# Kernel tuning notes

Measured on AMD Instinct MI355X. Metric: run time of the kernel, lower is better.

Reference implementation:

```python
import jax, jax.numpy as jnp
from jax import lax
import numpy as np

WIN = 9          # window size per spatial dim (default [9]*ndims)
PAD = WIN // 2
EPS = 1e-07


def _box_sum(x, groups):
    # depthwise conv with all-ones kernel == sliding-window sum
    kernel = jnp.ones((groups, 1, WIN, WIN), dtype=x.dtype)
    return lax.conv_general_dilated(
        x, kernel,
        window_strides=(1, 1),
        padding=[(PAD, PAD), (PAD, PAD)],
        feature_group_count=groups,
        dimension_numbers=('NCHW', 'OIHW', 'NCHW'))


def setup_inputs() -> dict:
    key = jax.random.key(0)
    k1, k2 = jax.random.split(key)
    shape = (8, 1, 1024, 1024)
    y_pred = jax.random.normal(k1, shape, dtype=jnp.float32)
    y_true = jax.random.normal(k2, shape, dtype=jnp.float32)
    return {"y_pred": y_pred, "y_true": y_true}


def reference(y_pred, y_true):
    Ii = y_true
    Ji = y_pred
    groups = Ii.shape[1]
    win_size = float(WIN * WIN)

    I_sum = _box_sum(Ii, groups)
    J_sum = _box_sum(Ji, groups)
    I2_sum = _box_sum(Ii * Ii, groups)
    J2_sum = _box_sum(Ji * Ji, groups)
    IJ_sum = _box_sum(Ii * Ji, groups)

    u_I = I_sum / win_size
    u_J = J_sum / win_size
    cross = IJ_sum / win_size - u_I * u_J
    I_var = I2_sum / win_size - u_I * u_I
    J_var = J2_sum / win_size - u_J * u_J

    cc = cross / jnp.sqrt(jnp.maximum(I_var * J_var, EPS))
    return 1.0 - jnp.mean(cc)
```

## Files before the change

### kernel.cpp

```cpp
#include <hip/hip_runtime.h>

#define H 1024
#define W 1024
#define TY 8
#define NT 64
#define RS 10
#define PCOL 264
#define NBK 64

__global__ void ncc_zero(double* acc) {
    if (threadIdx.x < NBK) acc[threadIdx.x] = 0.0;
}

__global__ void ncc_finalize(const double* __restrict__ acc, float* __restrict__ out) {
    double s = 0.0;
    #pragma unroll
    for (int i = 0; i < NBK; ++i) s += acc[i];
    out[0] = 1.0f - (float)(s * (1.0 / 8388608.0));
}

__device__ __forceinline__ unsigned pk2(float lo, float hi) {
    unsigned r;
    asm("v_cvt_pk_bf16_f32 %0, %1, %2" : "=v"(r) : "v"(lo), "v"(hi));
    return r;
}
__device__ __forceinline__ float ulo(unsigned u) { return __uint_as_float(u << 16); }
__device__ __forceinline__ float uhi(unsigned u) { return __uint_as_float(u & 0xffff0000u); }

__global__ __launch_bounds__(NT) void ncc_main(
    const float* __restrict__ Jg,
    const float* __restrict__ Ig,
    double* __restrict__ acc)
{
    __shared__ unsigned short ring[RS][2][PCOL];

    const int n     = blockIdx.x;
    const int b     = n & 7;
    const int rest  = n >> 3;
    const int panel = rest & 3;
    const int strip = rest >> 2;
    const int y0    = strip * TY;
    const int lane  = threadIdx.x;
    const int wb    = panel << 8;
    const int x0    = wb + (lane << 2);
    const int p0    = lane << 2;
    const int pown  = p0 + 4;

    const float* __restrict__ Ib = Ig + (size_t)b * (H * W);
    const float* __restrict__ Jb = Jg + (size_t)b * (H * W);

    const bool  hl  = (lane < 4);
    const int   hx  = (lane < 2) ? (wb - 4) : (wb + 256);
    const float mhx = (hl && (unsigned)hx <= (unsigned)(W - 4)) ? 1.0f : 0.0f;
    const int   hxc = min(max(hx, 0), W - 4);
    const float* hbase = (lane & 1) ? Jb : Ib;
    const int   hp  = (lane < 2) ? 0 : 260;
    const int   him = lane & 1;

    float rI[4]={0,0,0,0}, rJ[4]={0,0,0,0}, rII[4]={0,0,0,0}, rJJ[4]={0,0,0,0}, rIJ[4]={0,0,0,0};
    float accv = 0.0f;
    const float inv = 1.0f / 81.0f;

    float4 Pi, Pj, Ph = {0, 0, 0, 0};
    float  Pm;

#define FLOAD(yy) do {                                                              \
        const int r_ = (yy);                                                        \
        Pm = ((unsigned)r_ < (unsigned)H) ? 1.0f : 0.0f;                            \
        const int rc_ = min(max(r_, 0), H - 1);                                     \
        Pi = *(const float4*)(Ib + (size_t)rc_ * W + x0);                           \
        Pj = *(const float4*)(Jb + (size_t)rc_ * W + x0);                           \
        if (hl) Ph = *(const float4*)(hbase + (size_t)rc_ * W + hxc);               \
    } while (0)

#define PACKW(sl) do {                                                              \
        const unsigned i01_ = pk2(Pi.x * Pm, Pi.y * Pm);                            \
        const unsigned i23_ = pk2(Pi.z * Pm, Pi.w * Pm);                            \
        const unsigned j01_ = pk2(Pj.x * Pm, Pj.y * Pm);                            \
        const unsigned j23_ = pk2(Pj.z * Pm, Pj.w * Pm);                            \
        *(uint2*)&ring[sl][0][pown] = make_uint2(i01_, i23_);                       \
        *(uint2*)&ring[sl][1][pown] = make_uint2(j01_, j23_);                       \
        if (hl) {                                                                   \
            const float mm_ = Pm * mhx;                                             \
            const unsigned h01_ = pk2(Ph.x * mm_, Ph.y * mm_);                      \
            const unsigned h23_ = pk2(Ph.z * mm_, Ph.w * mm_);                      \
            *(uint2*)&ring[sl][him][hp] = make_uint2(h01_, h23_);                   \
        }                                                                           \
    } while (0)

#define READS(sl, A, B, C, D, E, F) do {                                            \
        A = *(const uint2*)&ring[sl][0][p0];                                        \
        B = *(const uint2*)&ring[sl][0][p0 + 4];                                    \
        C = *(const uint2*)&ring[sl][0][p0 + 8];                                    \
        D = *(const uint2*)&ring[sl][1][p0];                                        \
        E = *(const uint2*)&ring[sl][1][p0 + 4];                                    \
        F = *(const uint2*)&ring[sl][1][p0 + 8];                                    \
    } while (0)

#define FOLD12(Ua, Ub, Uc, Va, Vb, Vc, SG) do {                                     \
        const float i0=ulo(Ua.x), i1=uhi(Ua.x), i2=ulo(Ua.y), i3=uhi(Ua.y);         \
        const float i4=ulo(Ub.x), i5=uhi(Ub.x), i6=ulo(Ub.y), i7=uhi(Ub.y);         \
        const float i8=ulo(Uc.x), i9=uhi(Uc.x), i10=ulo(Uc.y), i11=uhi(Uc.y);       \
        const float j0=ulo(Va.x), j1=uhi(Va.x), j2=ulo(Va.y), j3=uhi(Va.y);         \
        const float j4=ulo(Vb.x), j5=uhi(Vb.x), j6=ulo(Vb.y), j7=uhi(Vb.y);         \
        const float j8=ulo(Vc.x), j9=uhi(Vc.x), j10=ulo(Vc.y), j11=uhi(Vc.y);       \
        { float s_ = i0+i1+i2+i3+i4+i5+i6+i7+i8;                                    \
          rI[0] += SG*s_; s_ += i9-i0;  rI[1] += SG*s_;                             \
          s_ += i10-i1;   rI[2] += SG*s_; s_ += i11-i2; rI[3] += SG*s_; }           \
        { float s_ = j0+j1+j2+j3+j4+j5+j6+j7+j8;                                    \
          rJ[0] += SG*s_; s_ += j9-j0;  rJ[1] += SG*s_;                             \
          s_ += j10-j1;   rJ[2] += SG*s_; s_ += j11-j2; rJ[3] += SG*s_; }           \
        { const float q0=i0*i0,q1=i1*i1,q2=i2*i2,q3=i3*i3,q4=i4*i4,q5=i5*i5;        \
          const float q6=i6*i6,q7=i7*i7,q8=i8*i8,q9=i9*i9,q10=i10*i10,q11=i11*i11;  \
          float s_ = q0+q1+q2+q3+q4+q5+q6+q7+q8;                                    \
          rII[0] += SG*s_; s_ += q9-q0;  rII[1] += SG*s_;                           \
          s_ += q10-q1;    rII[2] += SG*s_; s_ += q11-q2; rII[3] += SG*s_; }        \
        { const float q0=j0*j0,q1=j1*j1,q2=j2*j2,q3=j3*j3,q4=j4*j4,q5=j5*j5;        \
          const float q6=j6*j6,q7=j7*j7,q8=j8*j8,q9=j9*j9,q10=j10*j10,q11=j11*j11;  \
          float s_ = q0+q1+q2+q3+q4+q5+q6+q7+q8;                                    \
          rJJ[0] += SG*s_; s_ += q9-q0;  rJJ[1] += SG*s_;                           \
          s_ += q10-q1;    rJJ[2] += SG*s_; s_ += q11-q2; rJJ[3] += SG*s_; }        \
        { const float q0=i0*j0,q1=i1*j1,q2=i2*j2,q3=i3*j3,q4=i4*j4,q5=i5*j5;        \
          const float q6=i6*j6,q7=i7*j7,q8=i8*j8,q9=i9*j9,q10=i10*j10,q11=i11*j11;  \
          float s_ = q0+q1+q2+q3+q4+q5+q6+q7+q8;                                    \
          rIJ[0] += SG*s_; s_ += q9-q0;  rIJ[1] += SG*s_;                           \
          s_ += q10-q1;    rIJ[2] += SG*s_; s_ += q11-q2; rIJ[3] += SG*s_; }        \
    } while (0)

#define CC() do {                                                                   \
        _Pragma("unroll")                                                           \
        for (int c = 0; c < 4; ++c) {                                               \
            const float uI    = rI[c] * inv;                                        \
            const float uJ    = rJ[c] * inv;                                        \
            const float cross = rIJ[c] * inv - uI * uJ;                             \
            const float Iv    = rII[c] * inv - uI * uI;                             \
            const float Jv    = rJJ[c] * inv - uJ * uJ;                             \
            accv += cross * rsqrtf(fmaxf(Iv * Jv, 1e-7f));                          \
        }                                                                           \
    } while (0)

    FLOAD(y0 - 4);
    #pragma unroll 1
    for (int r = 0; r < 9; ++r) {
        PACKW(r);
        asm volatile("" ::: "memory");
        uint2 Ua, Ub, Uc, Va, Vb, Vc;
        READS(r, Ua, Ub, Uc, Va, Vb, Vc);
        asm volatile("" ::: "memory");
        FLOAD(y0 - 3 + r);
        FOLD12(Ua, Ub, Uc, Va, Vb, Vc, 1.0f);
    }

    int ls = 0, es = 9;
    #pragma unroll 1
    for (int k = 0; k < TY - 1; ++k) {
        PACKW(es);
        asm volatile("" ::: "memory");
        uint2 eUa, eUb, eUc, eVa, eVb, eVc;
        uint2 lUa, lUb, lUc, lVa, lVb, lVc;
        READS(es, eUa, eUb, eUc, eVa, eVb, eVc);
        READS(ls, lUa, lUb, lUc, lVa, lVb, lVc);
        asm volatile("" ::: "memory");
        FLOAD(y0 + 6 + k);
        CC();
        FOLD12(eUa, eUb, eUc, eVa, eVb, eVc,  1.0f);
        FOLD12(lUa, lUb, lUc, lVa, lVb, lVc, -1.0f);
        ls += 1;
        es = (es == RS - 1) ? 0 : es + 1;
    }
    CC();

#undef CC
#undef FOLD12
#undef READS
#undef PACKW
#undef FLOAD

    #pragma unroll
    for (int off = 32; off > 0; off >>= 1)
        accv += __shfl_down(accv, off);
    if (lane == 0)
        atomicAdd(&acc[n & (NBK - 1)], (double)accv);
}

extern "C" void kernel_launch(void* const* d_in, const int* in_sizes, int n_in,
                              void* d_out, int out_size, void* d_ws, size_t ws_size,
                              hipStream_t stream) {
    const float* y_pred = (const float*)d_in[0];
    const float* y_true = (const float*)d_in[1];
    float* out = (float*)d_out;
    double* accp = (double*)d_ws;

    ncc_zero<<<dim3(1), dim3(NBK), 0, stream>>>(accp);
    ncc_main<<<dim3(8 * 4 * (H / TY)), dim3(NT), 0, stream>>>(y_pred, y_true, accp);
    ncc_finalize<<<dim3(1), dim3(1), 0, stream>>>(accp, out);
}
```

Before: 46.25 us.

## Interleave I/J bf16 in uint4 LDS groups and double rows per block

Each ring slot now packs the I and J bf16 values for four columns into one uint4. A thread reads its 12-column window with three 16-byte LDS loads instead of six 8-byte loads, and each halo lane now loads both images. Rows per block go from 8 to 16, which halves the fraction of 9-row warm-up reads and folds per output row. The leaving-row index now wraps around the ring, which the longer loop needs. The trade-off is half as many blocks and a longer serial loop per wavefront.

```diff
diff --git a/kernel.cpp b/kernel.cpp
--- a/kernel.cpp
+++ b/kernel.cpp
@@ -2,10 +2,10 @@
 
 #define H 1024
 #define W 1024
-#define TY 8
+#define TY 16
 #define NT 64
 #define RS 10
-#define PCOL 264
+#define NG 66
 #define NBK 64
 
 __global__ void ncc_zero(double* acc) {
@@ -32,7 +32,7 @@
     const float* __restrict__ Ig,
     double* __restrict__ acc)
 {
-    __shared__ unsigned short ring[RS][2][PCOL];
+    __shared__ uint4 ring[RS][NG];
 
     const int n     = blockIdx.x;
     const int b     = n & 7;
@@ -43,25 +43,21 @@
     const int lane  = threadIdx.x;
     const int wb    = panel << 8;
     const int x0    = wb + (lane << 2);
-    const int p0    = lane << 2;
-    const int pown  = p0 + 4;
 
     const float* __restrict__ Ib = Ig + (size_t)b * (H * W);
     const float* __restrict__ Jb = Jg + (size_t)b * (H * W);
 
-    const bool  hl  = (lane < 4);
-    const int   hx  = (lane < 2) ? (wb - 4) : (wb + 256);
+    const bool  hl  = (lane < 2);
+    const int   hx  = (lane == 0) ? (wb - 4) : (wb + 256);
     const float mhx = (hl && (unsigned)hx <= (unsigned)(W - 4)) ? 1.0f : 0.0f;
     const int   hxc = min(max(hx, 0), W - 4);
-    const float* hbase = (lane & 1) ? Jb : Ib;
-    const int   hp  = (lane < 2) ? 0 : 260;
-    const int   him = lane & 1;
+    const int   hg  = (lane == 0) ? 0 : (NG - 1);
 
     float rI[4]={0,0,0,0}, rJ[4]={0,0,0,0}, rII[4]={0,0,0,0}, rJJ[4]={0,0,0,0}, rIJ[4]={0,0,0,0};
     float accv = 0.0f;
     const float inv = 1.0f / 81.0f;
 
-    float4 Pi, Pj, Ph = {0, 0, 0, 0};
+    float4 Pi, Pj, Phi = {0,0,0,0}, Phj = {0,0,0,0};
     float  Pm;
 
 #define FLOAD(yy) do {                                                              \
@@ -70,40 +66,43 @@
         const int rc_ = min(max(r_, 0), H - 1);                                     \
         Pi = *(const float4*)(Ib + (size_t)rc_ * W + x0);                           \
         Pj = *(const float4*)(Jb + (size_t)rc_ * W + x0);                           \
-        if (hl) Ph = *(const float4*)(hbase + (size_t)rc_ * W + hxc);               \
+        if (hl) {                                                                   \
+            Phi = *(const float4*)(Ib + (size_t)rc_ * W + hxc);                     \
+            Phj = *(const float4*)(Jb + (size_t)rc_ * W + hxc);                     \
+        }                                                                           \
     } while (0)
 
 #define PACKW(sl) do {                                                              \
-        const unsigned i01_ = pk2(Pi.x * Pm, Pi.y * Pm);                            \
-        const unsigned i23_ = pk2(Pi.z * Pm, Pi.w * Pm);                            \
-        const unsigned j01_ = pk2(Pj.x * Pm, Pj.y * Pm);                            \
-        const unsigned j23_ = pk2(Pj.z * Pm, Pj.w * Pm);                            \
-        *(uint2*)&ring[sl][0][pown] = make_uint2(i01_, i23_);                       \
-        *(uint2*)&ring[sl][1][pown] = make_uint2(j01_, j23_);                       \
+        uint4 v_;                                                                   \
+        v_.x = pk2(Pi.x * Pm, Pi.y * Pm);                                           \
+        v_.y = pk2(Pi.z * Pm, Pi.w * Pm);                                           \
+        v_.z = pk2(Pj.x * Pm, Pj.y * Pm);                                           \
+        v_.w = pk2(Pj.z * Pm, Pj.w * Pm);                                           \
+        ring[sl][lane + 1] = v_;                                                    \
         if (hl) {                                                                   \
             const float mm_ = Pm * mhx;                                             \
-            const unsigned h01_ = pk2(Ph.x * mm_, Ph.y * mm_);                      \
-            const unsigned h23_ = pk2(Ph.z * mm_, Ph.w * mm_);                      \
-            *(uint2*)&ring[sl][him][hp] = make_uint2(h01_, h23_);                   \
+            uint4 h_;                                                               \
+            h_.x = pk2(Phi.x * mm_, Phi.y * mm_);                                   \
+            h_.y = pk2(Phi.z * mm_, Phi.w * mm_);                                   \
+            h_.z = pk2(Phj.x * mm_, Phj.y * mm_);                                   \
+            h_.w = pk2(Phj.z * mm_, Phj.w * mm_);                                   \
+            ring[sl][hg] = h_;                                                      \
         }                                                                           \
     } while (0)
 
-#define READS(sl, A, B, C, D, E, F) do {                                            \
-        A = *(const uint2*)&ring[sl][0][p0];                                        \
-        B = *(const uint2*)&ring[sl][0][p0 + 4];                                    \
-        C = *(const uint2*)&ring[sl][0][p0 + 8];                                    \
-        D = *(const uint2*)&ring[sl][1][p0];                                        \
-        E = *(const uint2*)&ring[sl][1][p0 + 4];                                    \
-        F = *(const uint2*)&ring[sl][1][p0 + 8];                                    \
+#define READS(sl, G0, G1, G2) do {                                                  \
+        G0 = ring[sl][lane];                                                        \
+        G1 = ring[sl][lane + 1];                                                    \
+        G2 = ring[sl][lane + 2];                                                    \
     } while (0)
 
-#define FOLD12(Ua, Ub, Uc, Va, Vb, Vc, SG) do {                                     \
-        const float i0=ulo(Ua.x), i1=uhi(Ua.x), i2=ulo(Ua.y), i3=uhi(Ua.y);         \
-        const float i4=ulo(Ub.x), i5=uhi(Ub.x), i6=ulo(Ub.y), i7=uhi(Ub.y);         \
-        const float i8=ulo(Uc.x), i9=uhi(Uc.x), i10=ulo(Uc.y), i11=uhi(Uc.y);       \
-        const float j0=ulo(Va.x), j1=uhi(Va.x), j2=ulo(Va.y), j3=uhi(Va.y);         \
-        const float j4=ulo(Vb.x), j5=uhi(Vb.x), j6=ulo(Vb.y), j7=uhi(Vb.y);         \
-        const float j8=ulo(Vc.x), j9=uhi(Vc.x), j10=ulo(Vc.y), j11=uhi(Vc.y);       \
+#define FOLD12(G0, G1, G2, SG) do {                                                 \
+        const float i0=ulo(G0.x), i1=uhi(G0.x), i2=ulo(G0.y), i3=uhi(G0.y);         \
+        const float i4=ulo(G1.x), i5=uhi(G1.x), i6=ulo(G1.y), i7=uhi(G1.y);         \
+        const float i8=ulo(G2.x), i9=uhi(G2.x), i10=ulo(G2.y), i11=uhi(G2.y);       \
+        const float j0=ulo(G0.z), j1=uhi(G0.z), j2=ulo(G0.w), j3=uhi(G0.w);         \
+        const float j4=ulo(G1.z), j5=uhi(G1.z), j6=ulo(G1.w), j7=uhi(G1.w);         \
+        const float j8=ulo(G2.z), j9=uhi(G2.z), j10=ulo(G2.w), j11=uhi(G2.w);       \
         { float s_ = i0+i1+i2+i3+i4+i5+i6+i7+i8;                                    \
           rI[0] += SG*s_; s_ += i9-i0;  rI[1] += SG*s_;                             \
           s_ += i10-i1;   rI[2] += SG*s_; s_ += i11-i2; rI[3] += SG*s_; }           \
@@ -144,11 +143,11 @@
     for (int r = 0; r < 9; ++r) {
         PACKW(r);
         asm volatile("" ::: "memory");
-        uint2 Ua, Ub, Uc, Va, Vb, Vc;
-        READS(r, Ua, Ub, Uc, Va, Vb, Vc);
+        uint4 G0, G1, G2;
+        READS(r, G0, G1, G2);
         asm volatile("" ::: "memory");
         FLOAD(y0 - 3 + r);
-        FOLD12(Ua, Ub, Uc, Va, Vb, Vc, 1.0f);
+        FOLD12(G0, G1, G2, 1.0f);
     }
 
     int ls = 0, es = 9;
@@ -156,16 +155,15 @@
     for (int k = 0; k < TY - 1; ++k) {
         PACKW(es);
         asm volatile("" ::: "memory");
-        uint2 eUa, eUb, eUc, eVa, eVb, eVc;
-        uint2 lUa, lUb, lUc, lVa, lVb, lVc;
-        READS(es, eUa, eUb, eUc, eVa, eVb, eVc);
-        READS(ls, lUa, lUb, lUc, lVa, lVb, lVc);
+        uint4 e0, e1, e2, l0, l1, l2;
+        READS(es, e0, e1, e2);
+        READS(ls, l0, l1, l2);
         asm volatile("" ::: "memory");
         FLOAD(y0 + 6 + k);
         CC();
-        FOLD12(eUa, eUb, eUc, eVa, eVb, eVc,  1.0f);
-        FOLD12(lUa, lUb, lUc, lVa, lVb, lVc, -1.0f);
-        ls += 1;
+        FOLD12(e0, e1, e2,  1.0f);
+        FOLD12(l0, l1, l2, -1.0f);
+        ls = (ls == RS - 1) ? 0 : ls + 1;
         es = (es == RS - 1) ? 0 : es + 1;
     }
     CC();
```

After: 43.64 us. -5.6%, faster.
